# Optimization experiments

Measured on AMD Instinct MI355X. Metric: run time of the kernel, lower is better.

Reference implementation:

```python
import jax, jax.numpy as jnp
import numpy as np

D_CUT = 5.0   # cosine-cutoff distance
SIZE = 128    # rbf size == hidden_channels (nn_dist size = in_channels)
L = 2         # num_layers
EPS = 0.0     # GIN eps (non-trainable, initial 0)


def _rbf(d):
    # d: (E,) distances -> (E, SIZE) expnorm RBF with cosine cutoff
    d = d[:, None]
    start = float(np.exp(-D_CUT))
    means = jnp.linspace(start, 1.0, SIZE)
    beta = (2.0 / SIZE * (1.0 - start)) ** (-2)
    dc = jnp.minimum(d, D_CUT)
    cutoff = 0.5 * (jnp.cos(dc * jnp.pi / D_CUT) + 1.0)
    return cutoff * jnp.exp(-beta * (jnp.exp(-d) - means) ** 2)


def setup_inputs() -> dict:
    key = jax.random.key(0)
    ks = jax.random.split(key, 40)
    it = iter(range(40))
    def k():
        return ks[next(it)]
    N, H, ED, AS = 100000, 128, 4, 4
    def w(shape, s):
        return jax.random.normal(k(), shape, jnp.float32) * s
    inp = {}
    inp['x_lig'] = jax.random.normal(k(), (N, H), jnp.float32)
    inp['x_pock'] = jax.random.normal(k(), (N, H), jnp.float32)
    for name, E in (('bond', 200000), ('lp', 400000), ('pl', 400000)):
        inp['ei_' + name] = jax.random.randint(k(), (2, E), 0, N, jnp.int32)
        inp['ew_' + name] = jax.random.uniform(k(), (E,), jnp.float32) * D_CUT
        inp['ea_' + name] = jax.random.normal(k(), (E, AS), jnp.float32)
    inp['W0'] = w((3, AS, ED), 0.5)                 # initial per-edge-type lins (no bias)
    inp['Wd'] = w((L, 3, H, 2 * H), H ** -0.5)      # RBFDistanceScaleShift lin
    inp['bd'] = jnp.zeros((L, 3, 2 * H), jnp.float32)
    inp['We'] = w((L, 3, ED, H), 0.5)               # EGINConv.lin (edge_dim -> hidden)
    inp['be'] = jnp.zeros((L, 3, H), jnp.float32)
    inp['W1'] = w((L, 3, H, H), H ** -0.5)          # nn_node MLP layer 1
    inp['b1'] = jnp.zeros((L, 3, H), jnp.float32)
    inp['W2'] = w((L, 3, H, H), H ** -0.5)          # nn_node MLP layer 2
    inp['b2'] = jnp.zeros((L, 3, H), jnp.float32)
    return inp


def reference(x_lig, x_pock, ei_bond, ew_bond, ea_bond, ei_lp, ew_lp, ea_lp,
              ei_pl, ew_pl, ea_pl, W0, Wd, bd, We, be, W1, b1, W2, b2):
    # HeteroEGIN.forward: initial per-edge-type linear on raw edge attrs (bias-free)
    ea0 = ea_bond @ W0[0]
    ea1 = ea_lp @ W0[1]
    ea2 = ea_pl @ W0[2]

    def conv(x_src, x_dst, ei, ew, ea, t, l):
        # EGINConv per edge type t, layer l
        ss = _rbf(ew) @ Wd[l, t] + bd[l, t]            # (E, 2H) scale/shift from distance
        scale, shift = jnp.split(ss, 2, axis=1)
        xj = x_src[ei[0]] + (ea @ We[l, t] + be[l, t])  # gather + edge-attr lin
        msg = jax.nn.relu(xj * scale + shift)           # gated message
        agg = jax.ops.segment_sum(msg, ei[1], num_segments=x_dst.shape[0])
        o = agg + (1.0 + EPS) * x_dst
        return jax.nn.relu(o @ W1[l, t] + b1[l, t]) @ W2[l, t] + b2[l, t]

    for l in range(L):
        # to_hetero: sum conv outputs across edge types per destination node type
        new_lig = (conv(x_lig, x_lig, ei_bond, ew_bond, ea0, 0, l)
                   + conv(x_pock, x_lig, ei_pl, ew_pl, ea2, 2, l))
        new_pock = conv(x_lig, x_pock, ei_lp, ew_lp, ea1, 1, l)
        if l < L - 1:  # BasicGNN: act between layers, none after last (jk=None)
            new_lig = jax.nn.relu(new_lig)
            new_pock = jax.nn.relu(new_pock)
        x_lig, x_pock = new_lig, new_pock
    return jnp.concatenate([x_lig, x_pock], axis=0)
```

## Files before the change

kernel.cpp:

```cpp
#include <hip/hip_runtime.h>
#include <hip/hip_bf16.h>
#include <hip/hip_fp16.h>
#include <cmath>

typedef __attribute__((ext_vector_type(8))) short short8_t;
typedef __attribute__((ext_vector_type(4))) float f32x4;

static __device__ __forceinline__ short f2bs(float f) {
    union { __hip_bfloat16 h; short s; } u;
    u.h = __float2bfloat16(f);
    return u.s;
}
static __device__ __forceinline__ float bs2f(unsigned int us) {
    union { float f; unsigned int i; } u;
    u.i = us << 16;
    return u.f;
}
static __device__ __forceinline__ unsigned int pack2bf(float a, float b) {
    return (unsigned int)(unsigned short)f2bs(a) |
           ((unsigned int)(unsigned short)f2bs(b) << 16);
}
static __device__ __forceinline__ void lds_barrier() {
    asm volatile("s_waitcnt lgkmcnt(0)\n\ts_barrier" ::: "memory");
}

__global__ void pack_kernel(const float* __restrict__ Wd,
                            const float* __restrict__ W1,
                            const float* __restrict__ W2,
                            const float* __restrict__ W0,
                            const float* __restrict__ We,
                            short* __restrict__ pWd,
                            short* __restrict__ pW1,
                            short* __restrict__ pW2,
                            float* __restrict__ Mb)
{
    const int tid = blockIdx.x * blockDim.x + threadIdx.x;
    const int stride = gridDim.x * blockDim.x;
    for (int i = tid; i < 6 * 32768; i += stride) {
        int c = i >> 15, rem = i & 32767;
        int f = rem >> 9, l = (rem >> 3) & 63, j = rem & 7;
        int kk = f >> 4, nt = f & 15;
        int k = kk * 32 + (l >> 4) * 8 + j;
        int n = nt * 16 + (l & 15);
        pWd[i] = f2bs(Wd[(size_t)c * 32768 + k * 256 + n]);
    }
    for (int i = tid; i < 6 * 16384; i += stride) {
        int c = i >> 14, rem = i & 16383;
        int f = rem >> 9, l = (rem >> 3) & 63, j = rem & 7;
        int kk = f >> 3, nt = f & 7;
        int k = kk * 32 + (l >> 4) * 8 + j;
        int n = nt * 16 + (l & 15);
        pW1[i] = f2bs(W1[(size_t)c * 16384 + k * 128 + n]);
        pW2[i] = f2bs(W2[(size_t)c * 16384 + k * 128 + n]);
    }
    for (int i = tid; i < 6 * 512; i += stride) {
        int c = i >> 9, rem = i & 511;
        int a = rem >> 7, h = rem & 127;
        int t = c % 3;
        float m = 0.f;
        #pragma unroll
        for (int j = 0; j < 4; ++j)
            m = fmaf(W0[t * 16 + a * 4 + j], We[(size_t)c * 512 + j * 128 + h], m);
        Mb[i] = m;
    }
}

__global__ void tobf16_kernel(const float* __restrict__ a, const float* __restrict__ b,
                              unsigned short* __restrict__ oa, unsigned short* __restrict__ ob,
                              int n4)
{
    int i = blockIdx.x * blockDim.x + threadIdx.x;
    const int stride = gridDim.x * blockDim.x;
    for (; i < n4; i += stride) {
        float4 va = ((const float4*)a)[i];
        uint2 pa; pa.x = pack2bf(va.x, va.y); pa.y = pack2bf(va.z, va.w);
        ((uint2*)oa)[i] = pa;
        float4 vb = ((const float4*)b)[i];
        uint2 pb; pb.x = pack2bf(vb.x, vb.y); pb.y = pack2bf(vb.z, vb.w);
        ((uint2*)ob)[i] = pb;
    }
}

__global__ void hist3_kernel(const int* __restrict__ eiB, const int* __restrict__ eiL,
                             const int* __restrict__ eiP,
                             int EB, int EL, int EP, int N, int* __restrict__ cnt3)
{
    const int total = EB + EL + EP;
    for (int e = blockIdx.x * blockDim.x + threadIdx.x; e < total;
         e += gridDim.x * blockDim.x) {
        int base, le; const int* ei; int E;
        if (e < EB)           { base = 0;     le = e;           ei = eiB; E = EB; }
        else if (e < EB + EL) { base = N;     le = e - EB;      ei = eiL; E = EL; }
        else                  { base = 2 * N; le = e - EB - EL; ei = eiP; E = EP; }
        atomicAdd(&cnt3[base + ei[E + le]], 1);
    }
}

__global__ void scan1k_kernel(int* __restrict__ data, int* __restrict__ bsum, int n)
{
    __shared__ int buf[1024];
    const int gid = blockIdx.x * 1024 + threadIdx.x;
    int v = (gid < n) ? data[gid] : 0;
    buf[threadIdx.x] = v;
    __syncthreads();
    for (int off = 1; off < 1024; off <<= 1) {
        int t = (threadIdx.x >= off) ? buf[threadIdx.x - off] : 0;
        __syncthreads();
        buf[threadIdx.x] += t;
        __syncthreads();
    }
    if (gid < n) data[gid] = buf[threadIdx.x] - v;
    if (bsum && threadIdx.x == 1023) bsum[blockIdx.x] = buf[1023];
}

__global__ void scan_add_kernel(int* __restrict__ data, const int* __restrict__ bsum,
                                int* __restrict__ cursor, int n)
{
    const int gid = blockIdx.x * 1024 + threadIdx.x;
    if (gid < n) {
        int v = data[gid] + bsum[blockIdx.x];
        data[gid] = v;
        cursor[gid] = v;
    }
}

__global__ void scatter3_kernel(const int* __restrict__ eiB, const float* __restrict__ ewB,
                                const float4* __restrict__ eaB,
                                const int* __restrict__ eiL, const float* __restrict__ ewL,
                                const float4* __restrict__ eaL,
                                const int* __restrict__ eiP, const float* __restrict__ ewP,
                                const float4* __restrict__ eaP,
                                int EB, int EL, int EP, int N,
                                int* __restrict__ cursor,
                                uint4* __restrict__ rec, float* __restrict__ ewp)
{
    const int total = EB + EL + EP;
    for (int e = blockIdx.x * blockDim.x + threadIdx.x; e < total;
         e += gridDim.x * blockDim.x) {
        int base, le; const int* ei; const float* ew; const float4* ea; int E;
        if (e < EB)           { base = 0;     le = e;           ei = eiB; ew = ewB; ea = eaB; E = EB; }
        else if (e < EB + EL) { base = N;     le = e - EB;      ei = eiL; ew = ewL; ea = eaL; E = EL; }
        else                  { base = 2 * N; le = e - EB - EL; ei = eiP; ew = ewP; ea = eaP; E = EP; }
        int d = ei[E + le];
        int p = atomicAdd(&cursor[base + d], 1);
        float4 a = ea[le];
        uint4 r;
        r.x = (unsigned int)ei[le];
        r.y = (unsigned int)d;
        r.z = pack2bf(a.x, a.y);
        r.w = pack2bf(a.z, a.w);
        rec[p] = r;
        ewp[p] = ew[le];
    }
}

__global__ __launch_bounds__(512, 2)
void edge_mfma_kernel(
    const unsigned short* __restrict__ xsb,
    const uint4* __restrict__ rec,
    const float* __restrict__ ewp,
    const short* __restrict__ pWd, const float* __restrict__ bd,
    const float* __restrict__ Mb, const float* __restrict__ be,
    __half2* __restrict__ agg, int E, int ntiles,
    float rs, float rstep, float rbeta)
{
    __shared__ short sRbf[64 * 128];
    __shared__ __half sSS[64 * 256];

    const int t = threadIdx.x;
    const int lane = t & 63;
    const int w = t >> 6;
    const int l15 = lane & 15;
    const int l4 = lane >> 4;

    short8_t bfrag[4][2];
    #pragma unroll
    for (int kk = 0; kk < 4; ++kk)
        #pragma unroll
        for (int i = 0; i < 2; ++i)
            bfrag[kk][i] = *(const short8_t*)&pWd[((kk * 16 + 2 * w + i) * 64 + lane) * 8];
    float bdv[2];
    #pragma unroll
    for (int i = 0; i < 2; ++i) bdv[i] = bd[(2 * w + i) * 16 + l15];
    const float be0 = be[2 * lane], be1 = be[2 * lane + 1];
    float ma0[4], ma1[4];
    #pragma unroll
    for (int a = 0; a < 4; ++a) {
        ma0[a] = Mb[a * 128 + 2 * lane];
        ma1[a] = Mb[a * 128 + 2 * lane + 1];
    }

    const int stride = gridDim.x;
    int tile = blockIdx.x;
    if (tile >= ntiles) return;

    float ew_c; int src_c, dst_c; unsigned int ea01_c, ea23_c;
    unsigned int gx[8];
    {
        int eL = (tile << 6) + lane;
        int ec = eL < E ? eL : E - 1;
        uint4 r = rec[ec];
        ew_c = ewp[ec];
        src_c = (int)r.x;
        dst_c = (eL < E) ? (int)r.y : -1;
        ea01_c = r.z; ea23_c = r.w;
        #pragma unroll
        for (int rr = 0; rr < 8; ++rr) {
            int srn = __shfl(src_c, 8 * w + rr);
            gx[rr] = *(const unsigned int*)&xsb[(size_t)srn * 128 + lane * 2];
        }
    }

    for (; tile < ntiles; tile += stride) {
        const float edv = __expf(-ew_c);
        const float dcc = fminf(ew_c, 5.0f);
        const float cutv = 0.5f * (__cosf(dcc * 0.62831853071795864769f) + 1.0f);
        {
            char* base = (char*)sRbf + lane * 256;
            #pragma unroll
            for (int c = 0; c < 2; ++c) {
                short8_t v;
                #pragma unroll
                for (int j = 0; j < 8; ++j) {
                    float mean = rs + (float)(w * 16 + c * 8 + j) * rstep;
                    float diff = edv - mean;
                    v[j] = f2bs(cutv * __expf(-rbeta * diff * diff));
                }
                *(short8_t*)(base + ((w * 32 + c * 16) ^ ((lane & 7) << 4))) = v;
            }
        }
        unsigned int xjr[8];
        #pragma unroll
        for (int r = 0; r < 8; ++r) {
            unsigned int a01 = __shfl(ea01_c, 8 * w + r);
            unsigned int a23 = __shfl(ea23_c, 8 * w + r);
            float ea0 = bs2f(a01 & 0xffffu), ea1 = bs2f(a01 >> 16);
            float ea2 = bs2f(a23 & 0xffffu), ea3 = bs2f(a23 >> 16);
            unsigned int g = gx[r];
            float x0 = bs2f(g & 0xffffu), x1 = bs2f(g >> 16);
            float o0 = x0 + be0 + ea0 * ma0[0] + ea1 * ma0[1] + ea2 * ma0[2] + ea3 * ma0[3];
            float o1 = x1 + be1 + ea0 * ma1[0] + ea1 * ma1[1] + ea2 * ma1[2] + ea3 * ma1[3];
            xjr[r] = pack2bf(o0, o1);
        }

        lds_barrier();

        const int ntile = tile + stride;
        const bool has_next = ntile < ntiles;
        float ew_n = 0.f; int src_n = 0, dst_n = -1;
        unsigned int ea01_n = 0, ea23_n = 0;
        if (has_next) {
            int eL = (ntile << 6) + lane;
            int ec = eL < E ? eL : E - 1;
            uint4 r = rec[ec];
            ew_n = ewp[ec];
            src_n = (int)r.x;
            dst_n = (eL < E) ? (int)r.y : -1;
            ea01_n = r.z; ea23_n = r.w;
        }
        __builtin_amdgcn_sched_barrier(0);

        f32x4 acc[4][2];
        #pragma unroll
        for (int m = 0; m < 4; ++m) {
            acc[m][0] = (f32x4){0.f, 0.f, 0.f, 0.f};
            acc[m][1] = (f32x4){0.f, 0.f, 0.f, 0.f};
        }
        #pragma unroll
        for (int kk = 0; kk < 4; ++kk) {
            short8_t af[4];
            #pragma unroll
            for (int m = 0; m < 4; ++m) {
                int row = m * 16 + l15;
                int byte = row * 256 + ((kk * 64 + l4 * 16) ^ ((row & 7) << 4));
                af[m] = *(const short8_t*)((const char*)sRbf + byte);
            }
            #pragma unroll
            for (int m = 0; m < 4; ++m)
                #pragma unroll
                for (int i = 0; i < 2; ++i)
                    acc[m][i] = __builtin_amdgcn_mfma_f32_16x16x32_bf16(
                        af[m], bfrag[kk][i], acc[m][i], 0, 0, 0);
        }

        #pragma unroll
        for (int m = 0; m < 4; ++m)
            #pragma unroll
            for (int i = 0; i < 2; ++i) {
                int col = (2 * w + i) * 16 + l15;
                #pragma unroll
                for (int r = 0; r < 4; ++r) {
                    int row = m * 16 + l4 * 4 + r;
                    int byte = row * 512 + ((col * 2) ^ ((row & 7) << 4));
                    *(__half*)((char*)sSS + byte) = __float2half(acc[m][i][r] + bdv[i]);
                }
            }

        if (has_next) {
            #pragma unroll
            for (int r = 0; r < 8; ++r) {
                int srn = __shfl(src_n, 8 * w + r);
                gx[r] = *(const unsigned int*)&xsb[(size_t)srn * 128 + lane * 2];
            }
        }
        const int dst_f = dst_c;
        ew_c = ew_n; src_c = src_n; dst_c = dst_n; ea01_c = ea01_n; ea23_c = ea23_n;

        lds_barrier();

        {
            float a0 = 0.f, a1 = 0.f;
            int rdst = __shfl(dst_f, 8 * w);
            #pragma unroll
            for (int r = 0; r < 8; ++r) {
                int e = 8 * w + r;
                unsigned int sc = *(const unsigned int*)
                    ((const char*)sSS + e * 512 + ((lane * 4) ^ ((e & 7) << 4)));
                unsigned int sh = *(const unsigned int*)
                    ((const char*)sSS + e * 512 + ((256 + lane * 4) ^ ((e & 7) << 4)));
                float2 scf = __half22float2(*(const __half2*)&sc);
                float2 shf = __half22float2(*(const __half2*)&sh);
                unsigned int g = xjr[r];
                float x0 = bs2f(g & 0xffffu), x1 = bs2f(g >> 16);
                float m0 = fmaxf(fmaf(x0, scf.x, shf.x), 0.0f);
                float m1 = fmaxf(fmaf(x1, scf.y, shf.y), 0.0f);
                int d = __shfl(dst_f, e);
                if (d != rdst) {
                    if (rdst >= 0) {
                        __half2 hv = __floats2half2_rn(a0, a1);
                        unsigned int hb;
                        __builtin_memcpy(&hb, &hv, 4);
                        if (hb)
                            unsafeAtomicAdd(agg + (size_t)rdst * 64 + lane, hv);
                    }
                    a0 = 0.f; a1 = 0.f; rdst = d;
                }
                a0 += m0; a1 += m1;
            }
            if (rdst >= 0) {
                __half2 hv = __floats2half2_rn(a0, a1);
                unsigned int hb;
                __builtin_memcpy(&hb, &hv, 4);
                if (hb)
                    unsafeAtomicAdd(agg + (size_t)rdst * 64 + lane, hv);
            }
        }
    }
}

__global__ __launch_bounds__(256)
void node_mfma_kernel(
    __half2* __restrict__ agg,
    const float* __restrict__ xdf, const unsigned short* __restrict__ xdb,
    const short* __restrict__ pW1, const float* __restrict__ b1,
    const short* __restrict__ pW2, const float* __restrict__ b2,
    float* __restrict__ outf, unsigned short* __restrict__ outb,
    int N, int ntiles, int accumulate, int relu_out)
{
    __shared__ short sA[64 * 128];
    __shared__ short sH[64 * 128];

    const int t = threadIdx.x;
    const int lane = t & 63;
    const int w = t >> 6;
    const int l15 = lane & 15;
    const int l4 = lane >> 4;

    short8_t w1f[4][2], w2f[4][2];
    #pragma unroll
    for (int kk = 0; kk < 4; ++kk)
        #pragma unroll
        for (int p = 0; p < 2; ++p) {
            int nt = 2 * w + p;
            w1f[kk][p] = *(const short8_t*)&pW1[((kk * 8 + nt) * 64 + lane) * 8];
            w2f[kk][p] = *(const short8_t*)&pW2[((kk * 8 + nt) * 64 + lane) * 8];
        }
    float b1v[2], b2v[2];
    #pragma unroll
    for (int p = 0; p < 2; ++p) {
        int col = (2 * w + p) * 16 + l15;
        b1v[p] = b1[col];
        b2v[p] = b2[col];
    }

    const float4 zero4 = {0.f, 0.f, 0.f, 0.f};

    for (int tile = blockIdx.x; tile < ntiles; tile += gridDim.x) {
        const int n0 = tile << 6;
        #pragma unroll
        for (int i = 0; i < 4; ++i) {
            int idx = i * 256 + t;
            int row = idx >> 4, c8 = idx & 15;
            int gr = n0 + row; if (gr >= N) gr = N - 1;
            union { float4 f; __half2 h[4]; } ar;
            ar.f = ((const float4*)agg)[(size_t)gr * 16 + c8];
            ((float4*)agg)[(size_t)gr * 16 + c8] = zero4;
            float xv[8];
            if (xdf) {
                float4 x0 = ((const float4*)xdf)[(size_t)gr * 32 + c8 * 2];
                float4 x1 = ((const float4*)xdf)[(size_t)gr * 32 + c8 * 2 + 1];
                xv[0] = x0.x; xv[1] = x0.y; xv[2] = x0.z; xv[3] = x0.w;
                xv[4] = x1.x; xv[5] = x1.y; xv[6] = x1.z; xv[7] = x1.w;
            } else {
                uint4 xr = ((const uint4*)xdb)[(size_t)gr * 16 + c8];
                xv[0] = bs2f(xr.x & 0xffffu); xv[1] = bs2f(xr.x >> 16);
                xv[2] = bs2f(xr.y & 0xffffu); xv[3] = bs2f(xr.y >> 16);
                xv[4] = bs2f(xr.z & 0xffffu); xv[5] = bs2f(xr.z >> 16);
                xv[6] = bs2f(xr.w & 0xffffu); xv[7] = bs2f(xr.w >> 16);
            }
            short8_t v;
            #pragma unroll
            for (int j = 0; j < 4; ++j) {
                float2 a2 = __half22float2(ar.h[j]);
                v[2 * j]     = f2bs(a2.x + xv[2 * j]);
                v[2 * j + 1] = f2bs(a2.y + xv[2 * j + 1]);
            }
            int byte = row * 256 + ((c8 * 16) ^ ((row & 7) << 4));
            *(short8_t*)((char*)sA + byte) = v;
        }
        lds_barrier();

        f32x4 acc[4][2];
        #pragma unroll
        for (int m = 0; m < 4; ++m) {
            acc[m][0] = (f32x4){0.f, 0.f, 0.f, 0.f};
            acc[m][1] = (f32x4){0.f, 0.f, 0.f, 0.f};
        }
        #pragma unroll
        for (int kk = 0; kk < 4; ++kk) {
            short8_t af[4];
            #pragma unroll
            for (int m = 0; m < 4; ++m) {
                int row = m * 16 + l15;
                int byte = row * 256 + ((kk * 64 + l4 * 16) ^ ((row & 7) << 4));
                af[m] = *(const short8_t*)((const char*)sA + byte);
            }
            #pragma unroll
            for (int m = 0; m < 4; ++m)
                #pragma unroll
                for (int p = 0; p < 2; ++p)
                    acc[m][p] = __builtin_amdgcn_mfma_f32_16x16x32_bf16(
                        af[m], w1f[kk][p], acc[m][p], 0, 0, 0);
        }
        #pragma unroll
        for (int m = 0; m < 4; ++m)
            #pragma unroll
            for (int p = 0; p < 2; ++p) {
                int col = (2 * w + p) * 16 + l15;
                #pragma unroll
                for (int r = 0; r < 4; ++r) {
                    int row = m * 16 + l4 * 4 + r;
                    short hs = f2bs(fmaxf(acc[m][p][r] + b1v[p], 0.f));
                    int byte = row * 256 + ((col * 2) ^ ((row & 7) << 4));
                    *(short*)((char*)sH + byte) = hs;
                }
            }
        lds_barrier();

        f32x4 acc2[4][2];
        #pragma unroll
        for (int m = 0; m < 4; ++m) {
            acc2[m][0] = (f32x4){0.f, 0.f, 0.f, 0.f};
            acc2[m][1] = (f32x4){0.f, 0.f, 0.f, 0.f};
        }
        #pragma unroll
        for (int kk = 0; kk < 4; ++kk) {
            short8_t af[4];
            #pragma unroll
            for (int m = 0; m < 4; ++m) {
                int row = m * 16 + l15;
                int byte = row * 256 + ((kk * 64 + l4 * 16) ^ ((row & 7) << 4));
                af[m] = *(const short8_t*)((const char*)sH + byte);
            }
            #pragma unroll
            for (int m = 0; m < 4; ++m)
                #pragma unroll
                for (int p = 0; p < 2; ++p)
                    acc2[m][p] = __builtin_amdgcn_mfma_f32_16x16x32_bf16(
                        af[m], w2f[kk][p], acc2[m][p], 0, 0, 0);
        }
        #pragma unroll
        for (int m = 0; m < 4; ++m)
            #pragma unroll
            for (int p = 0; p < 2; ++p) {
                int col = (2 * w + p) * 16 + l15;
                #pragma unroll
                for (int r = 0; r < 4; ++r) {
                    int row = n0 + m * 16 + l4 * 4 + r;
                    if (row < N) {
                        float v = acc2[m][p][r] + b2v[p];
                        if (outf) {
                            float* op = &outf[(size_t)row * 128 + col];
                            if (accumulate) v += *op;
                            if (relu_out) v = fmaxf(v, 0.f);
                            *op = v;
                        } else {
                            unsigned short* op = &outb[(size_t)row * 128 + col];
                            if (accumulate) v += bs2f((unsigned int)*op);
                            if (relu_out) v = fmaxf(v, 0.f);
                            *op = (unsigned short)f2bs(v);
                        }
                    }
                }
            }
    }
}

extern "C" void kernel_launch(void* const* d_in, const int* in_sizes, int n_in,
                              void* d_out, int out_size, void* d_ws, size_t ws_size,
                              hipStream_t stream)
{
    const float* x_lig   = (const float*)d_in[0];
    const float* x_pock  = (const float*)d_in[1];
    const int*   ei_bond = (const int*)d_in[2];
    const float* ew_bond = (const float*)d_in[3];
    const float* ea_bond = (const float*)d_in[4];
    const int*   ei_lp   = (const int*)d_in[5];
    const float* ew_lp   = (const float*)d_in[6];
    const float* ea_lp   = (const float*)d_in[7];
    const int*   ei_pl   = (const int*)d_in[8];
    const float* ew_pl   = (const float*)d_in[9];
    const float* ea_pl   = (const float*)d_in[10];
    const float* W0 = (const float*)d_in[11];
    const float* Wd = (const float*)d_in[12];
    const float* bd = (const float*)d_in[13];
    const float* We = (const float*)d_in[14];
    const float* be = (const float*)d_in[15];
    const float* W1 = (const float*)d_in[16];
    const float* b1 = (const float*)d_in[17];
    const float* W2 = (const float*)d_in[18];
    const float* b2 = (const float*)d_in[19];

    const int H = 128;
    const int N = in_sizes[0] / H;
    const int E_bond = in_sizes[3];
    const int E_lp   = in_sizes[6];
    const int E_pl   = in_sizes[9];
    const int E_all  = E_bond + E_lp + E_pl;

    char* wp = (char*)d_ws;
    auto alloc = [&](size_t bytes) -> char* {
        char* r = wp;
        wp += (bytes + 255) & ~(size_t)255;
        return r;
    };
    unsigned short* A   = (unsigned short*)alloc((size_t)N * H * 2);
    unsigned short* Bb  = (unsigned short*)alloc((size_t)N * H * 2);
    unsigned short* C   = (unsigned short*)alloc((size_t)N * H * 2);
    __half*  agg  = (__half*)alloc((size_t)N * H * 2);
    int*     cnt3 = (int*)alloc((size_t)3 * N * 4);
    char*    zero_end = wp;
    uint4*   recAll = (uint4*)alloc((size_t)E_all * 16);
    float*   ewpAll = (float*)alloc((size_t)E_all * 4);
    short*   pWd  = (short*)alloc(6 * 32768 * 2);
    short*   pW1s = (short*)alloc(6 * 16384 * 2);
    short*   pW2s = (short*)alloc(6 * 16384 * 2);
    float*   Mb   = (float*)alloc(6 * 512 * 4);
    int*     cursor = (int*)alloc((size_t)3 * N * 4);
    int*     bsum   = (int*)alloc(1024 * 4);

    const uint4* recB = recAll;
    const uint4* recL = recAll + E_bond;
    const uint4* recP = recAll + E_bond + E_lp;
    const float* ewpB = ewpAll;
    const float* ewpL = ewpAll + E_bond;
    const float* ewpP = ewpAll + E_bond + E_lp;

    float* outL = (float*)d_out;
    float* outP = outL + (size_t)N * H;

    const int capE = 256;
    const int capN = 4 * 256;

    hipMemsetAsync(agg, 0, (size_t)(zero_end - (char*)agg), stream);
    tobf16_kernel<<<512, 256, 0, stream>>>(x_lig, x_pock, A, Bb, N * H / 4);
    pack_kernel<<<256, 256, 0, stream>>>(Wd, W1, W2, W0, We, pWd, pW1s, pW2s, Mb);

    const int n3 = 3 * N;
    const int nb3 = (n3 + 1023) / 1024;
    hist3_kernel<<<1024, 256, 0, stream>>>(ei_bond, ei_lp, ei_pl,
                                           E_bond, E_lp, E_pl, N, cnt3);
    scan1k_kernel<<<nb3, 1024, 0, stream>>>(cnt3, bsum, n3);
    scan1k_kernel<<<1, 1024, 0, stream>>>(bsum, nullptr, nb3);
    scan_add_kernel<<<nb3, 1024, 0, stream>>>(cnt3, bsum, cursor, n3);
    scatter3_kernel<<<1024, 256, 0, stream>>>(
        ei_bond, ew_bond, (const float4*)ea_bond,
        ei_lp,   ew_lp,   (const float4*)ea_lp,
        ei_pl,   ew_pl,   (const float4*)ea_pl,
        E_bond, E_lp, E_pl, N, cursor, recAll, ewpAll);

    const double start_d = exp(-5.0);
    const float rs    = (float)start_d;
    const float rstep = (float)((1.0 - start_d) / 127.0);
    const float rbeta = (float)std::pow(2.0 / 128.0 * (1.0 - start_d), -2.0);

    auto conv = [&](const unsigned short* src,
                    const float* xdf, const unsigned short* xdb,
                    const uint4* rec, const float* ewp, int E,
                    int l, int tt, float* outf, unsigned short* outb,
                    int accum, int relu) {
        const int lt = l * 3 + tt;
        const int ntE = (E + 63) / 64;
        const int gE = ntE < capE ? ntE : capE;
        edge_mfma_kernel<<<gE, 512, 0, stream>>>(
            src, rec, ewp,
            pWd + (size_t)lt * 32768, bd + (size_t)lt * 256,
            Mb + (size_t)lt * 512, be + (size_t)lt * 128,
            (__half2*)agg, E, ntE, rs, rstep, rbeta);
        const int ntN = (N + 63) / 64;
        const int gN = ntN < capN ? ntN : capN;
        node_mfma_kernel<<<gN, 256, 0, stream>>>(
            (__half2*)agg, xdf, xdb,
            pW1s + (size_t)lt * 16384, b1 + (size_t)lt * 128,
            pW2s + (size_t)lt * 16384, b2 + (size_t)lt * 128,
            outf, outb, N, ntN, accum, relu);
    };

    conv(A,  x_pock, nullptr, recL, ewpL, E_lp,   0, 1, nullptr, C, 0, 1);
    conv(A,  x_lig,  nullptr, recB, ewpB, E_bond, 0, 0, nullptr, A, 0, 0);
    conv(Bb, x_lig,  nullptr, recP, ewpP, E_pl,   0, 2, nullptr, A, 1, 1);
    conv(A, nullptr, A, recB, ewpB, E_bond, 1, 0, outL, nullptr, 0, 0);
    conv(C, nullptr, A, recP, ewpP, E_pl,   1, 2, outL, nullptr, 1, 0);
    conv(A, nullptr, C, recL, ewpL, E_lp,   1, 1, outP, nullptr, 0, 0);
}
```

Before: 812.0 us.

## Deepen edge-kernel prefetch pipeline to two tiles ahead and relax occupancy bound

Edge records are now loaded two tiles ahead, and the x-row gathers for the next tile are issued before the MFMA section instead of after it. This gives the dependent gather loads more time to land under the RBF matmul. Launch bounds drop the min-2-blocks hint, which lets the compiler use more registers for the extra prefetch state. The cost is higher register pressure and possibly lower occupancy.

```diff
diff --git a/kernel.cpp b/kernel.cpp
--- a/kernel.cpp
+++ b/kernel.cpp
@@ -154,7 +154,7 @@
     }
 }
 
-__global__ __launch_bounds__(512, 2)
+__global__ __launch_bounds__(512)
 void edge_mfma_kernel(
     const unsigned short* __restrict__ xsb,
     const uint4* __restrict__ rec,
@@ -195,6 +195,7 @@
     if (tile >= ntiles) return;
 
     float ew_c; int src_c, dst_c; unsigned int ea01_c, ea23_c;
+    float ew_n; int src_n, dst_n; unsigned int ea01_n, ea23_n;
     unsigned int gx[8];
     {
         int eL = (tile << 6) + lane;
@@ -208,6 +209,17 @@
         for (int rr = 0; rr < 8; ++rr) {
             int srn = __shfl(src_c, 8 * w + rr);
             gx[rr] = *(const unsigned int*)&xsb[(size_t)srn * 128 + lane * 2];
+        }
+        int t1 = tile + stride;
+        ew_n = 0.f; src_n = 0; dst_n = -1; ea01_n = 0; ea23_n = 0;
+        if (t1 < ntiles) {
+            int eL1 = (t1 << 6) + lane;
+            int ec1 = eL1 < E ? eL1 : E - 1;
+            uint4 r1 = rec[ec1];
+            ew_n = ewp[ec1];
+            src_n = (int)r1.x;
+            dst_n = (eL1 < E) ? (int)r1.y : -1;
+            ea01_n = r1.z; ea23_n = r1.w;
         }
     }
 
@@ -245,18 +257,25 @@
 
         lds_barrier();
 
-        const int ntile = tile + stride;
-        const bool has_next = ntile < ntiles;
-        float ew_n = 0.f; int src_n = 0, dst_n = -1;
-        unsigned int ea01_n = 0, ea23_n = 0;
-        if (has_next) {
-            int eL = (ntile << 6) + lane;
+        const bool has_n1 = tile + stride < ntiles;
+        const bool has_n2 = tile + 2 * stride < ntiles;
+        if (has_n1) {
+            #pragma unroll
+            for (int r = 0; r < 8; ++r) {
+                int srn = __shfl(src_n, 8 * w + r);
+                gx[r] = *(const unsigned int*)&xsb[(size_t)srn * 128 + lane * 2];
+            }
+        }
+        float ew_n2 = 0.f; int src_n2 = 0, dst_n2 = -1;
+        unsigned int ea01_n2 = 0, ea23_n2 = 0;
+        if (has_n2) {
+            int eL = ((tile + 2 * stride) << 6) + lane;
             int ec = eL < E ? eL : E - 1;
             uint4 r = rec[ec];
-            ew_n = ewp[ec];
-            src_n = (int)r.x;
-            dst_n = (eL < E) ? (int)r.y : -1;
-            ea01_n = r.z; ea23_n = r.w;
+            ew_n2 = ewp[ec];
+            src_n2 = (int)r.x;
+            dst_n2 = (eL < E) ? (int)r.y : -1;
+            ea01_n2 = r.z; ea23_n2 = r.w;
         }
         __builtin_amdgcn_sched_barrier(0);
 
@@ -296,21 +315,11 @@
                 }
             }
 
-        if (has_next) {
-            #pragma unroll
-            for (int r = 0; r < 8; ++r) {
-                int srn = __shfl(src_n, 8 * w + r);
-                gx[r] = *(const unsigned int*)&xsb[(size_t)srn * 128 + lane * 2];
-            }
-        }
-        const int dst_f = dst_c;
-        ew_c = ew_n; src_c = src_n; dst_c = dst_n; ea01_c = ea01_n; ea23_c = ea23_n;
-
         lds_barrier();
 
         {
             float a0 = 0.f, a1 = 0.f;
-            int rdst = __shfl(dst_f, 8 * w);
+            int rdst = __shfl(dst_c, 8 * w);
             #pragma unroll
             for (int r = 0; r < 8; ++r) {
                 int e = 8 * w + r;
@@ -324,7 +333,7 @@
                 float x0 = bs2f(g & 0xffffu), x1 = bs2f(g >> 16);
                 float m0 = fmaxf(fmaf(x0, scf.x, shf.x), 0.0f);
                 float m1 = fmaxf(fmaf(x1, scf.y, shf.y), 0.0f);
-                int d = __shfl(dst_f, e);
+                int d = __shfl(dst_c, e);
                 if (d != rdst) {
                     if (rdst >= 0) {
                         __half2 hv = __floats2half2_rn(a0, a1);
@@ -345,6 +354,9 @@
                     unsafeAtomicAdd(agg + (size_t)rdst * 64 + lane, hv);
             }
         }
+
+        ew_c = ew_n;  src_c = src_n;  dst_c = dst_n;  ea01_c = ea01_n;  ea23_c = ea23_n;
+        ew_n = ew_n2; src_n = src_n2; dst_n = dst_n2; ea01_n = ea01_n2; ea23_n = ea23_n2;
     }
 }
 
```

Measured after the change: 841.3 us. 3.6% more time.

## Process 128 edges per tile in edge MFMA kernel to amortize weight fragments

Applied to the files above, without the earlier changes.

The edge kernel now handles 128 edges per block iteration instead of 64. Each wave owns 16 edges for gather and scatter, the MFMA loop runs 8 M-blocks against the same register-resident Wd fragments, and the per-tile barriers are amortized over twice the work. LDS use doubles to 96 KB, and the launch bound drops the two-blocks-per-CU hint. That raises register pressure and likely lowers occupancy, reducing latency hiding for the gathers and atomics.

```diff
diff --git a/kernel.cpp b/kernel.cpp
--- a/kernel.cpp
+++ b/kernel.cpp
@@ -154,7 +154,7 @@
     }
 }
 
-__global__ __launch_bounds__(512, 2)
+__global__ __launch_bounds__(512)
 void edge_mfma_kernel(
     const unsigned short* __restrict__ xsb,
     const uint4* __restrict__ rec,
@@ -164,14 +164,15 @@
     __half2* __restrict__ agg, int E, int ntiles,
     float rs, float rstep, float rbeta)
 {
-    __shared__ short sRbf[64 * 128];
-    __shared__ __half sSS[64 * 256];
+    __shared__ short sRbf[128 * 128];
+    __shared__ __half sSS[128 * 256];
 
     const int t = threadIdx.x;
     const int lane = t & 63;
     const int w = t >> 6;
     const int l15 = lane & 15;
     const int l4 = lane >> 4;
+    const bool loHalf = (w < 4);
 
     short8_t bfrag[4][2];
     #pragma unroll
@@ -194,46 +195,63 @@
     int tile = blockIdx.x;
     if (tile >= ntiles) return;
 
-    float ew_c; int src_c, dst_c; unsigned int ea01_c, ea23_c;
-    unsigned int gx[8];
+    float ew_c0, ew_c1; int src_c0, src_c1, dst_c0, dst_c1;
+    unsigned int ea01_c0, ea01_c1, ea23_c0, ea23_c1;
+    unsigned int gx[16];
     {
-        int eL = (tile << 6) + lane;
-        int ec = eL < E ? eL : E - 1;
-        uint4 r = rec[ec];
-        ew_c = ewp[ec];
-        src_c = (int)r.x;
-        dst_c = (eL < E) ? (int)r.y : -1;
-        ea01_c = r.z; ea23_c = r.w;
-        #pragma unroll
-        for (int rr = 0; rr < 8; ++rr) {
-            int srn = __shfl(src_c, 8 * w + rr);
-            gx[rr] = *(const unsigned int*)&xsb[(size_t)srn * 128 + lane * 2];
+        int eL0 = (tile << 7) + lane;
+        int ec0 = eL0 < E ? eL0 : E - 1;
+        uint4 r0 = rec[ec0];
+        ew_c0 = ewp[ec0];
+        src_c0 = (int)r0.x;
+        dst_c0 = (eL0 < E) ? (int)r0.y : -1;
+        ea01_c0 = r0.z; ea23_c0 = r0.w;
+        int eL1 = eL0 + 64;
+        int ec1 = eL1 < E ? eL1 : E - 1;
+        uint4 r1 = rec[ec1];
+        ew_c1 = ewp[ec1];
+        src_c1 = (int)r1.x;
+        dst_c1 = (eL1 < E) ? (int)r1.y : -1;
+        ea01_c1 = r1.z; ea23_c1 = r1.w;
+        #pragma unroll
+        for (int r = 0; r < 16; ++r) {
+            int eloc = (16 * w + r) & 63;
+            int srn = loHalf ? __shfl(src_c0, eloc) : __shfl(src_c1, eloc);
+            gx[r] = *(const unsigned int*)&xsb[(size_t)srn * 128 + lane * 2];
         }
     }
 
     for (; tile < ntiles; tile += stride) {
-        const float edv = __expf(-ew_c);
-        const float dcc = fminf(ew_c, 5.0f);
-        const float cutv = 0.5f * (__cosf(dcc * 0.62831853071795864769f) + 1.0f);
         {
-            char* base = (char*)sRbf + lane * 256;
-            #pragma unroll
-            for (int c = 0; c < 2; ++c) {
-                short8_t v;
+            const float edv0 = __expf(-ew_c0);
+            const float cut0 = 0.5f * (__cosf(fminf(ew_c0, 5.0f) * 0.62831853071795864769f) + 1.0f);
+            const float edv1 = __expf(-ew_c1);
+            const float cut1 = 0.5f * (__cosf(fminf(ew_c1, 5.0f) * 0.62831853071795864769f) + 1.0f);
+            #pragma unroll
+            for (int h = 0; h < 2; ++h) {
+                const float edv = h ? edv1 : edv0;
+                const float cutv = h ? cut1 : cut0;
+                const int e = h * 64 + lane;
+                char* base = (char*)sRbf + e * 256;
                 #pragma unroll
-                for (int j = 0; j < 8; ++j) {
-                    float mean = rs + (float)(w * 16 + c * 8 + j) * rstep;
-                    float diff = edv - mean;
-                    v[j] = f2bs(cutv * __expf(-rbeta * diff * diff));
+                for (int c = 0; c < 2; ++c) {
+                    short8_t v;
+                    #pragma unroll
+                    for (int j = 0; j < 8; ++j) {
+                        float mean = rs + (float)(w * 16 + c * 8 + j) * rstep;
+                        float diff = edv - mean;
+                        v[j] = f2bs(cutv * __expf(-rbeta * diff * diff));
+                    }
+                    *(short8_t*)(base + ((w * 32 + c * 16) ^ ((e & 7) << 4))) = v;
                 }
-                *(short8_t*)(base + ((w * 32 + c * 16) ^ ((lane & 7) << 4))) = v;
-            }
-        }
-        unsigned int xjr[8];
-        #pragma unroll
-        for (int r = 0; r < 8; ++r) {
-            unsigned int a01 = __shfl(ea01_c, 8 * w + r);
-            unsigned int a23 = __shfl(ea23_c, 8 * w + r);
+            }
+        }
+        unsigned int xjr[16];
+        #pragma unroll
+        for (int r = 0; r < 16; ++r) {
+            int eloc = (16 * w + r) & 63;
+            unsigned int a01 = loHalf ? __shfl(ea01_c0, eloc) : __shfl(ea01_c1, eloc);
+            unsigned int a23 = loHalf ? __shfl(ea23_c0, eloc) : __shfl(ea23_c1, eloc);
             float ea0 = bs2f(a01 & 0xffffu), ea1 = bs2f(a01 >> 16);
             float ea2 = bs2f(a23 & 0xffffu), ea3 = bs2f(a23 >> 16);
             unsigned int g = gx[r];
@@ -247,36 +265,44 @@
 
         const int ntile = tile + stride;
         const bool has_next = ntile < ntiles;
-        float ew_n = 0.f; int src_n = 0, dst_n = -1;
-        unsigned int ea01_n = 0, ea23_n = 0;
+        float ew_n0 = 0.f, ew_n1 = 0.f;
+        int src_n0 = 0, src_n1 = 0, dst_n0 = -1, dst_n1 = -1;
+        unsigned int ea01_n0 = 0, ea01_n1 = 0, ea23_n0 = 0, ea23_n1 = 0;
         if (has_next) {
-            int eL = (ntile << 6) + lane;
-            int ec = eL < E ? eL : E - 1;
-            uint4 r = rec[ec];
-            ew_n = ewp[ec];
-            src_n = (int)r.x;
-            dst_n = (eL < E) ? (int)r.y : -1;
-            ea01_n = r.z; ea23_n = r.w;
+            int eL0 = (ntile << 7) + lane;
+            int ec0 = eL0 < E ? eL0 : E - 1;
+            uint4 r0 = rec[ec0];
+            ew_n0 = ewp[ec0];
+            src_n0 = (int)r0.x;
+            dst_n0 = (eL0 < E) ? (int)r0.y : -1;
+            ea01_n0 = r0.z; ea23_n0 = r0.w;
+            int eL1 = eL0 + 64;
+            int ec1 = eL1 < E ? eL1 : E - 1;
+            uint4 r1 = rec[ec1];
+            ew_n1 = ewp[ec1];
+            src_n1 = (int)r1.x;
+            dst_n1 = (eL1 < E) ? (int)r1.y : -1;
+            ea01_n1 = r1.z; ea23_n1 = r1.w;
         }
         __builtin_amdgcn_sched_barrier(0);
 
-        f32x4 acc[4][2];
-        #pragma unroll
-        for (int m = 0; m < 4; ++m) {
+        f32x4 acc[8][2];
+        #pragma unroll
+        for (int m = 0; m < 8; ++m) {
             acc[m][0] = (f32x4){0.f, 0.f, 0.f, 0.f};
             acc[m][1] = (f32x4){0.f, 0.f, 0.f, 0.f};
         }
         #pragma unroll
         for (int kk = 0; kk < 4; ++kk) {
-            short8_t af[4];
-            #pragma unroll
-            for (int m = 0; m < 4; ++m) {
+            short8_t af[8];
+            #pragma unroll
+            for (int m = 0; m < 8; ++m) {
                 int row = m * 16 + l15;
                 int byte = row * 256 + ((kk * 64 + l4 * 16) ^ ((row & 7) << 4));
                 af[m] = *(const short8_t*)((const char*)sRbf + byte);
             }
             #pragma unroll
-            for (int m = 0; m < 4; ++m)
+            for (int m = 0; m < 8; ++m)
                 #pragma unroll
                 for (int i = 0; i < 2; ++i)
                     acc[m][i] = __builtin_amdgcn_mfma_f32_16x16x32_bf16(
@@ -284,7 +310,7 @@
         }
 
         #pragma unroll
-        for (int m = 0; m < 4; ++m)
+        for (int m = 0; m < 8; ++m)
             #pragma unroll
             for (int i = 0; i < 2; ++i) {
                 int col = (2 * w + i) * 16 + l15;
@@ -298,22 +324,25 @@
 
         if (has_next) {
             #pragma unroll
-            for (int r = 0; r < 8; ++r) {
-                int srn = __shfl(src_n, 8 * w + r);
+            for (int r = 0; r < 16; ++r) {
+                int eloc = (16 * w + r) & 63;
+                int srn = loHalf ? __shfl(src_n0, eloc) : __shfl(src_n1, eloc);
                 gx[r] = *(const unsigned int*)&xsb[(size_t)srn * 128 + lane * 2];
             }
         }
-        const int dst_f = dst_c;
-        ew_c = ew_n; src_c = src_n; dst_c = dst_n; ea01_c = ea01_n; ea23_c = ea23_n;
+        const int dst_f0 = dst_c0, dst_f1 = dst_c1;
+        ew_c0 = ew_n0; src_c0 = src_n0; dst_c0 = dst_n0; ea01_c0 = ea01_n0; ea23_c0 = ea23_n0;
+        ew_c1 = ew_n1; src_c1 = src_n1; dst_c1 = dst_n1; ea01_c1 = ea01_n1; ea23_c1 = ea23_n1;
 
         lds_barrier();
 
         {
             float a0 = 0.f, a1 = 0.f;
-            int rdst = __shfl(dst_f, 8 * w);
-            #pragma unroll
-            for (int r = 0; r < 8; ++r) {
-                int e = 8 * w + r;
+            int rdst = loHalf ? __shfl(dst_f0, (16 * w) & 63)
+                              : __shfl(dst_f1, (16 * w) & 63);
+            #pragma unroll
+            for (int r = 0; r < 16; ++r) {
+                int e = 16 * w + r;
                 unsigned int sc = *(const unsigned int*)
                     ((const char*)sSS + e * 512 + ((lane * 4) ^ ((e & 7) << 4)));
                 unsigned int sh = *(const unsigned int*)
@@ -324,7 +353,7 @@
                 float x0 = bs2f(g & 0xffffu), x1 = bs2f(g >> 16);
                 float m0 = fmaxf(fmaf(x0, scf.x, shf.x), 0.0f);
                 float m1 = fmaxf(fmaf(x1, scf.y, shf.y), 0.0f);
-                int d = __shfl(dst_f, e);
+                int d = loHalf ? __shfl(dst_f0, e & 63) : __shfl(dst_f1, e & 63);
                 if (d != rdst) {
                     if (rdst >= 0) {
                         __half2 hv = __floats2half2_rn(a0, a1);
@@ -600,7 +629,7 @@
                     int l, int tt, float* outf, unsigned short* outb,
                     int accum, int relu) {
         const int lt = l * 3 + tt;
-        const int ntE = (E + 63) / 64;
+        const int ntE = (E + 127) / 128;
         const int gE = ntE < capE ? ntE : capE;
         edge_mfma_kernel<<<gE, 512, 0, stream>>>(
             src, rec, ewp,
```

Measured after the change: 2.265 ms. +178.9%, slower.
